# Optimization experiments

Hardware: AMD Instinct MI355X
Metric: run time of the kernel (lower is better)

## Reference

```python
import jax, jax.numpy as jnp
import numpy as np

B, S, D, H, DFF, NL, VOCAB, SRC = 16, 128, 768, 12, 3072, 6, 32000, 256


def _pe_table():
    pos = np.arange(S)[:, None].astype(np.float32)
    div = np.exp(np.arange(0, D, 2).astype(np.float32) * (-np.log(10000.0) / D))
    pe = np.zeros((S, D), np.float32)
    pe[:, 0::2] = np.sin(pos * div)
    pe[:, 1::2] = np.cos(pos * div)
    return jnp.asarray(pe)


def _ln(x, a, b, eps=1e-6):
    m = jnp.mean(x, axis=-1, keepdims=True)
    v = jnp.mean((x - m) ** 2, axis=-1, keepdims=True)
    return a * (x - m) / jnp.sqrt(v + eps) + b


def _mha(q_in, k_in, v_in, mask, Wq, bq, Wk, bk, Wv, bv, Wo, bo):
    Bq, Sq, Dm = q_in.shape
    Sk = k_in.shape[1]
    dk = Dm // H
    q = (q_in @ Wq + bq).reshape(Bq, Sq, H, dk).transpose(0, 2, 1, 3)
    k = (k_in @ Wk + bk).reshape(Bq, Sk, H, dk).transpose(0, 2, 1, 3)
    v = (v_in @ Wv + bv).reshape(Bq, Sk, H, dk).transpose(0, 2, 1, 3)
    s = jnp.einsum('bhqd,bhkd->bhqk', q, k) / jnp.sqrt(jnp.float32(dk))
    if mask is not None:
        s = jnp.where(mask == 0, jnp.float32(-1e9), s)
    a = jax.nn.softmax(s, axis=-1)
    o = jnp.einsum('bhqk,bhkd->bhqd', a, v).transpose(0, 2, 1, 3).reshape(Bq, Sq, Dm)
    return o @ Wo + bo


def _combined_mask(trg):
    # Vectorized, faithful replica of create_combined_mask (incl. its cumulative
    # cross-batch zeroing: for j in 0..B-2, if padding_start[j]!=0 zero rows
    # >= padding_start[j] of ALL batches b >= j).
    b, s = trg.shape
    is_pad = (trg == 0)
    haspad = jnp.any(is_pad, axis=1)
    start = jnp.where(haspad, jnp.argmax(is_pad, axis=1), 0)  # first pad idx, 0 if none
    c = jnp.where(start == 0, s + 1, start)                   # sentinel = never cut
    cmin = jax.lax.cummin(c)
    r = cmin[jnp.minimum(jnp.arange(b), b - 2)]               # effective cutoff per batch
    look = jnp.tril(jnp.ones((s, s), jnp.float32))
    keep = (jnp.arange(s)[None, :] < r[:, None]).astype(jnp.float32)  # (B,S) rows kept
    return (look[None] * keep[:, :, None])[:, None]           # (B,1,S,S)


def setup_inputs():
    key = jax.random.key(0)
    ks = jax.random.split(key, 16)
    tok = jax.random.randint(ks[0], (B, S), 1, VOCAB)
    lens = jax.random.randint(ks[1], (B,), S // 2, S + 1)
    trg = jnp.where(jnp.arange(S)[None, :] < lens[:, None], tok, 0).astype(jnp.int32)
    e_outputs = jax.random.normal(ks[2], (B, SRC, D), dtype=jnp.float32)
    src_mask = jax.random.randint(ks[3], (B, 1, 1, SRC), 0, 2).at[..., 0].set(1).astype(jnp.int32)
    w = lambda k, shape: (jax.random.normal(k, shape) * 0.02).astype(jnp.float32)
    emb = (jax.random.normal(ks[4], (VOCAB, D)) * 0.1).astype(jnp.float32).at[0].set(0.0)
    return {
        'trg': trg, 'e_outputs': e_outputs, 'src_mask': src_mask,
        'emb': emb,
        'y_param': jax.random.normal(ks[5], (S, D), dtype=jnp.float32),
        'pe_alpha': jnp.float32(1.0),
        'Wq': w(ks[6], (NL, 3, D, D)), 'Wk': w(ks[7], (NL, 3, D, D)),
        'Wv': w(ks[8], (NL, 3, D, D)), 'Wo': w(ks[9], (NL, 3, D, D)),
        'bq': jnp.zeros((NL, 3, D)), 'bk': jnp.zeros((NL, 3, D)),
        'bv': jnp.zeros((NL, 3, D)), 'bo': jnp.zeros((NL, 3, D)),
        'W1': w(ks[10], (NL, D, DFF)), 'b1': jnp.zeros((NL, DFF)),
        'W2': w(ks[11], (NL, DFF, D)), 'b2': jnp.zeros((NL, D)),
        'ln_a': jnp.ones((NL, 5, D)), 'ln_b': jnp.zeros((NL, 5, D)),
        'final_a': jnp.ones((D,)), 'final_b': jnp.zeros((D,)),
    }


def reference(trg, e_outputs, src_mask, emb, y_param, pe_alpha, Wq, Wk, Wv, Wo,
              bq, bk, bv, bo, W1, b1, W2, b2, ln_a, ln_b, final_a, final_b):
    x = emb[trg] + pe_alpha * _pe_table()            # embedding + scaled PE
    y = jnp.broadcast_to(y_param, (trg.shape[0],) + y_param.shape)
    trg_mask = _combined_mask(trg)
    for i in range(Wq.shape[0]):
        x2 = _ln(x, ln_a[i, 0], ln_b[i, 0])
        x = x + _mha(x2, x2, x2, trg_mask, Wq[i, 0], bq[i, 0], Wk[i, 0], bk[i, 0], Wv[i, 0], bv[i, 0], Wo[i, 0], bo[i, 0])
        y2 = _ln(y, ln_a[i, 1], ln_b[i, 1])
        y = y + _mha(y2, e_outputs, e_outputs, src_mask, Wq[i, 1], bq[i, 1], Wk[i, 1], bk[i, 1], Wv[i, 1], bv[i, 1], Wo[i, 1], bo[i, 1])
        x2 = _ln(x, ln_a[i, 2], ln_b[i, 2])
        y3 = _ln(y, ln_a[i, 3], ln_b[i, 3])
        x = x + _mha(x2, y3, y3, None, Wq[i, 2], bq[i, 2], Wk[i, 2], bk[i, 2], Wv[i, 2], bv[i, 2], Wo[i, 2], bo[i, 2])
        x2 = _ln(x, ln_a[i, 4], ln_b[i, 4])
        x = x + jnp.maximum(x2 @ W1[i] + b1[i], 0.0) @ W2[i] + b2[i]
    return _ln(x, final_a, final_b)
```

## Files before the change

kernel.cpp:

```cpp
#include <hip/hip_runtime.h>
#include <math.h>

#define BB 16
#define SS 128
#define DD 768
#define HH 12
#define DKK 64
#define DFFF 3072
#define NLL 6
#define SRCC 256

typedef short bf16x8 __attribute__((ext_vector_type(8)));
typedef float f32x4 __attribute__((ext_vector_type(4)));
typedef unsigned short us8 __attribute__((ext_vector_type(8)));
typedef unsigned short us4 __attribute__((ext_vector_type(4)));

__device__ __forceinline__ unsigned short f2bf(float f) {
  unsigned int u = __builtin_bit_cast(unsigned int, f);
  u = (u + 0x7fff + ((u >> 16) & 1)) >> 16;
  return (unsigned short)u;
}

#define GLOADLDS16(gp, lp)                                              \
  __builtin_amdgcn_global_load_lds(                                     \
      (const __attribute__((address_space(1))) void*)(gp),              \
      (__attribute__((address_space(3))) void*)(lp), 16, 0, 0)

__global__ void embjoint_k(const int* __restrict__ trg, const float* __restrict__ emb,
                           const float* __restrict__ alpha,
                           const float* __restrict__ yp,
                           float* __restrict__ x, float* __restrict__ y) {
  int idx = blockIdx.x * blockDim.x + threadIdx.x;
  int c = idx % (DD / 4);
  int r = idx / (DD / 4);
  if (r >= BB * SS) return;
  int s = r % SS;
  if (blockIdx.y == 0) {
    float al = alpha[0];
    float4 e = *(const float4*)(emb + (size_t)trg[r] * DD + c * 4);
    float coef = -logf(10000.0f) / (float)DD;
    float div0 = expf((float)(4 * c) * coef);
    float div1 = expf((float)(4 * c + 2) * coef);
    float s0, c0, s1, c1;
    sincosf((float)s * div0, &s0, &c0);
    sincosf((float)s * div1, &s1, &c1);
    float4 o;
    o.x = e.x + al * s0; o.y = e.y + al * c0;
    o.z = e.z + al * s1; o.w = e.w + al * c1;
    *(float4*)(x + (size_t)r * DD + c * 4) = o;
  } else {
    *(float4*)(y + (size_t)r * DD + c * 4) = *(const float4*)(yp + (size_t)s * DD + c * 4);
  }
}

__global__ void mb_k(const int* __restrict__ trg, int* __restrict__ rbuf,
                     const float* __restrict__ bq, const float* __restrict__ bk,
                     const float* __restrict__ bv, float* __restrict__ bqkv1,
                     float* __restrict__ bkv2, float* __restrict__ bqkv3) {
  int t = threadIdx.x;
  if (blockIdx.x == 0) {
    __shared__ int first[BB];
    if (t < BB) first[t] = 0x7fffffff;
    __syncthreads();
    int b = t >> 4, p0 = (t & 15) * 8;
    int loc = 0x7fffffff;
#pragma unroll
    for (int i = 0; i < 8; i++) {
      if (trg[b * SS + p0 + i] == 0) { loc = p0 + i; break; }
    }
    atomicMin(&first[b], loc);
    __syncthreads();
    if (t == 0) {
      int cmin = 0x7fffffff;
      int cm[BB];
      for (int bb = 0; bb < BB; bb++) {
        int start = (first[bb] == 0x7fffffff) ? 0 : first[bb];
        int c = (start == 0) ? (SS + 1) : start;
        cmin = min(cmin, c);
        cm[bb] = cmin;
      }
      for (int bb = 0; bb < BB; bb++) rbuf[bb] = cm[min(bb, BB - 2)];
    }
    return;
  }
  int i = (blockIdx.x - 1) * 256 + t;
  if (i >= NLL * 6144) return;
  int l = i / 6144, j = i - l * 6144;
  if (j < 2304) {
    int s = j / 768, c = j - s * 768;
    const float* src = (s == 0) ? bq : (s == 1 ? bk : bv);
    bqkv1[l * 2304 + j] = src[(l * 3 + 0) * 768 + c];
  } else if (j < 3840) {
    int jj = j - 2304;
    int s = jj / 768, c = jj - s * 768;
    bkv2[l * 1536 + jj] = ((s == 0) ? bk : bv)[(l * 3 + 1) * 768 + c];
  } else {
    int jj = j - 3840;
    int s = jj / 768, c = jj - s * 768;
    const float* src = (s == 0) ? bq : (s == 1 ? bk : bv);
    bqkv3[l * 2304 + jj] = src[(l * 3 + 2) * 768 + c];
  }
}

__global__ __launch_bounds__(256) void ln_k(const float* __restrict__ x,
                                            const float* __restrict__ ga,
                                            const float* __restrict__ gb,
                                            float* __restrict__ out) {
  __shared__ float sm[8];
  int row = blockIdx.x;
  int t = threadIdx.x;
  const float* xr = x + (size_t)row * DD;
  float v0 = xr[t], v1 = xr[t + 256], v2 = xr[t + 512];
  float s = v0 + v1 + v2;
#pragma unroll
  for (int o = 32; o > 0; o >>= 1) s += __shfl_down(s, o);
  if ((t & 63) == 0) sm[t >> 6] = s;
  __syncthreads();
  float mean = (sm[0] + sm[1] + sm[2] + sm[3]) * (1.0f / (float)DD);
  float d0 = v0 - mean, d1 = v1 - mean, d2 = v2 - mean;
  float q = d0 * d0 + d1 * d1 + d2 * d2;
#pragma unroll
  for (int o = 32; o > 0; o >>= 1) q += __shfl_down(q, o);
  if ((t & 63) == 0) sm[4 + (t >> 6)] = q;
  __syncthreads();
  float var = (sm[4] + sm[5] + sm[6] + sm[7]) * (1.0f / (float)DD);
  float inv = 1.0f / sqrtf(var + 1e-6f);
  float* orow = out + (size_t)row * DD;
  orow[t]       = ga[t] * d0 * inv + gb[t];
  orow[t + 256] = ga[t + 256] * d1 * inv + gb[t + 256];
  orow[t + 512] = ga[t + 512] * d2 * inv + gb[t + 512];
}

__device__ __forceinline__ void lnb_body(const float* __restrict__ xr,
                                         const float* __restrict__ ga,
                                         const float* __restrict__ gb,
                                         unsigned short* __restrict__ orow,
                                         float* sm, int t) {
  float v0 = xr[t], v1 = xr[t + 256], v2 = xr[t + 512];
  float s = v0 + v1 + v2;
#pragma unroll
  for (int o = 32; o > 0; o >>= 1) s += __shfl_down(s, o);
  if ((t & 63) == 0) sm[t >> 6] = s;
  __syncthreads();
  float mean = (sm[0] + sm[1] + sm[2] + sm[3]) * (1.0f / (float)DD);
  float d0 = v0 - mean, d1 = v1 - mean, d2 = v2 - mean;
  float q = d0 * d0 + d1 * d1 + d2 * d2;
#pragma unroll
  for (int o = 32; o > 0; o >>= 1) q += __shfl_down(q, o);
  if ((t & 63) == 0) sm[4 + (t >> 6)] = q;
  __syncthreads();
  float var = (sm[4] + sm[5] + sm[6] + sm[7]) * (1.0f / (float)DD);
  float inv = 1.0f / sqrtf(var + 1e-6f);
  orow[t]       = f2bf(ga[t] * d0 * inv + gb[t]);
  orow[t + 256] = f2bf(ga[t + 256] * d1 * inv + gb[t + 256]);
  orow[t + 512] = f2bf(ga[t + 512] * d2 * inv + gb[t + 512]);
}

__global__ __launch_bounds__(256) void lnb_k(const float* __restrict__ x,
                                             const float* __restrict__ ga,
                                             const float* __restrict__ gb,
                                             unsigned short* __restrict__ out) {
  __shared__ float sm[8];
  int row = blockIdx.x;
  lnb_body(x + (size_t)row * DD, ga, gb, out + (size_t)row * DD, sm, threadIdx.x);
}

__global__ __launch_bounds__(256) void lnb2_k(const float* __restrict__ x,
                                              const float* __restrict__ y,
                                              const float* __restrict__ gax,
                                              const float* __restrict__ gbx,
                                              const float* __restrict__ gay,
                                              const float* __restrict__ gby,
                                              unsigned short* __restrict__ ox,
                                              unsigned short* __restrict__ oy) {
  __shared__ float sm[8];
  int row = blockIdx.x;
  if (row < BB * SS)
    lnb_body(x + (size_t)row * DD, gax, gbx, ox + (size_t)row * DD, sm, threadIdx.x);
  else {
    row -= BB * SS;
    lnb_body(y + (size_t)row * DD, gay, gby, oy + (size_t)row * DD, sm, threadIdx.x);
  }
}

__device__ __forceinline__ void tr_tile(const float* __restrict__ s,
                                        unsigned short* __restrict__ d,
                                        int K, int N, int k0, int n0,
                                        float (*tl)[69], int t) {
#pragma unroll
  for (int i = 0; i < 8; i++) {
    int c = t + i * 256;
    int row = c >> 4, c4 = (c & 15) * 4;
    float4 v = *(const float4*)(s + (size_t)(k0 + row) * N + n0 + c4);
    tl[row][c4 + 0] = v.x; tl[row][c4 + 1] = v.y;
    tl[row][c4 + 2] = v.z; tl[row][c4 + 3] = v.w;
  }
  __syncthreads();
#pragma unroll
  for (int i = 0; i < 4; i++) {
    int c = t + i * 256;
    int n = c >> 4, kc = c & 15;
    us8 o;
#pragma unroll
    for (int j = 0; j < 8; j++) o[j] = f2bf(tl[kc * 8 + j][n]);
    *(us8*)(d + (size_t)(n0 + n) * K + k0 + kc * 8) = o;
  }
}

__global__ __launch_bounds__(256) void wtx_k(
    const float* __restrict__ Wq, const float* __restrict__ Wk,
    const float* __restrict__ Wv, const float* __restrict__ Wo,
    const float* __restrict__ W1, const float* __restrict__ W2,
    const float* __restrict__ e_out,
    unsigned short* __restrict__ wqkv1A, unsigned short* __restrict__ wq2A,
    unsigned short* __restrict__ wkv2A, unsigned short* __restrict__ wqkv3A,
    unsigned short* __restrict__ wotA,
    unsigned short* __restrict__ w1tA, unsigned short* __restrict__ w2tA,
    unsigned short* __restrict__ eob) {
  __shared__ float tl[128][69];
  const size_t M1 = (size_t)DD * DD;
  int bid = blockIdx.x;
  int t = threadIdx.x;
  if (bid < 5184) {
    int mat = bid / 72, rem = bid % 72;
    int kt = rem / 12, nt = rem % 12;
    int l = mat / 12, m = mat % 12;
    size_t s3 = (size_t)l * 3 * M1;
    const float* s;
    unsigned short* d;
    switch (m) {
      case 0:  s = Wq + s3;          d = wqkv1A + l * 3 * M1;          break;
      case 1:  s = Wk + s3;          d = wqkv1A + l * 3 * M1 + M1;     break;
      case 2:  s = Wv + s3;          d = wqkv1A + l * 3 * M1 + 2 * M1; break;
      case 3:  s = Wq + s3 + M1;     d = wq2A + l * M1;                break;
      case 4:  s = Wk + s3 + M1;     d = wkv2A + l * 2 * M1;           break;
      case 5:  s = Wv + s3 + M1;     d = wkv2A + l * 2 * M1 + M1;      break;
      case 6:  s = Wq + s3 + 2 * M1; d = wqkv3A + l * 3 * M1;          break;
      case 7:  s = Wk + s3 + 2 * M1; d = wqkv3A + l * 3 * M1 + M1;     break;
      case 8:  s = Wv + s3 + 2 * M1; d = wqkv3A + l * 3 * M1 + 2 * M1; break;
      case 9:  s = Wo + s3;          d = wotA + l * 3 * M1;            break;
      case 10: s = Wo + s3 + M1;     d = wotA + l * 3 * M1 + M1;       break;
      default: s = Wo + s3 + 2 * M1; d = wotA + l * 3 * M1 + 2 * M1;   break;
    }
    tr_tile(s, d, DD, DD, kt * 128, nt * 64, tl, t);
  } else if (bid < 6912) {
    int idx = bid - 5184;
    int l = idx / 288, rem = idx % 288;
    int kt = rem / 48, nt = rem % 48;
    tr_tile(W1 + (size_t)l * DD * DFFF, w1tA + (size_t)l * DD * DFFF,
            DD, DFFF, kt * 128, nt * 64, tl, t);
  } else if (bid < 8640) {
    int idx = bid - 6912;
    int l = idx / 288, rem = idx % 288;
    int kt = rem / 12, nt = rem % 12;
    tr_tile(W2 + (size_t)l * DFFF * DD, w2tA + (size_t)l * DFFF * DD,
            DFFF, DD, kt * 128, nt * 64, tl, t);
  } else {
    size_t base = (size_t)(bid - 8640) * 2048 + (size_t)t * 8;
    float4 a = *(const float4*)(e_out + base);
    float4 b = *(const float4*)(e_out + base + 4);
    us8 o;
    o[0] = f2bf(a.x); o[1] = f2bf(a.y); o[2] = f2bf(a.z); o[3] = f2bf(a.w);
    o[4] = f2bf(b.x); o[5] = f2bf(b.y); o[6] = f2bf(b.z); o[7] = f2bf(b.w);
    *(us8*)(eob + base) = o;
  }
}

#define GEMM_BODY(BM, A, Bt, m0, n0)                                          \
  constexpr int FM = (BM) / 32;                                               \
  constexpr int HB = (BM) / 2;                                                \
  int wave = t >> 6, lane = t & 63;                                           \
  int wm = wave >> 1, wn = wave & 1;                                          \
  f32x4 acc[FM][2] = {};                                                      \
  int aRow = t >> 2, aC8 = (t & 3) * 8;                                       \
  const unsigned short* Ab = (A) + (size_t)(m0)*768 + aC8;                    \
  const unsigned short* Bb = (Bt) + (size_t)(n0)*768 + aC8;                   \
  int aOff0 = (wm * HB + (lane & 15)) * 32 + (lane >> 4) * 8;                 \
  int bOff0 = (wn * 32 + (lane & 15)) * 32 + (lane >> 4) * 8;                 \
  for (int k0 = 0; k0 < 768; k0 += 32) {                                      \
    _Pragma("unroll")                                                         \
    for (int h = 0; h < (BM) / 64; h++)                                       \
      GLOADLDS16(Ab + (size_t)(h * 64 + aRow) * 768 + k0,                     \
                 As + h * 2048 + wave * 512);                                 \
    GLOADLDS16(Bb + (size_t)aRow * 768 + k0, Bs + wave * 512);                \
    __syncthreads();                                                          \
    bf16x8 aF[FM], bF[2];                                                     \
    _Pragma("unroll")                                                         \
    for (int fm = 0; fm < FM; fm++)                                           \
      aF[fm] = *(const bf16x8*)(As + aOff0 + fm * 16 * 32);                   \
    _Pragma("unroll")                                                         \
    for (int fn = 0; fn < 2; fn++)                                            \
      bF[fn] = *(const bf16x8*)(Bs + bOff0 + fn * 16 * 32);                   \
    _Pragma("unroll")                                                         \
    for (int fm = 0; fm < FM; fm++)                                           \
      _Pragma("unroll")                                                       \
      for (int fn = 0; fn < 2; fn++)                                          \
        acc[fm][fn] = __builtin_amdgcn_mfma_f32_16x16x32_bf16(                \
            aF[fm], bF[fn], acc[fm][fn], 0, 0, 0);                            \
    __syncthreads();                                                          \
  }                                                                           \
  int lcol = lane & 15, lrow4 = (lane >> 4) * 4;

__device__ __forceinline__ void hm_store(unsigned short* hd, int sh, int vt,
                                         int rowb, int colr, const f32x4& a,
                                         float bv) {
  int hh = colr >> 6, dd = colr & 63;
  int bb = rowb >> sh, ssb = rowb & ((1 << sh) - 1);
  if (vt) {
    size_t idx = (((size_t)bb * HH + hh) * 64 + dd) * (size_t)(1 << sh) + ssb;
    us4 pk;
#pragma unroll
    for (int r = 0; r < 4; r++) pk[r] = f2bf(a[r] + bv);
    *(us4*)(hd + idx) = pk;
  } else {
    size_t base = ((((size_t)bb * HH + hh) << sh) + ssb) * 64 + dd;
#pragma unroll
    for (int r = 0; r < 4; r++) hd[base + (size_t)r * 64] = f2bf(a[r] + bv);
  }
}

template <int BM>
__global__ __launch_bounds__(256) void mgemm_k(
    const unsigned short* __restrict__ A0, const unsigned short* __restrict__ A1,
    const unsigned short* __restrict__ Bt, const float* __restrict__ bias,
    const float* __restrict__ res, void* __restrict__ C,
    unsigned short* __restrict__ hd0, unsigned short* __restrict__ hd1,
    unsigned short* __restrict__ hd2,
    int sh0, int sh1, int sh2, int M, int N, int K, int flags, int vtbits) {
  constexpr int FM = BM / 32;
  constexpr int HB = BM / 2;
  __shared__ unsigned short As[BM * 32];
  __shared__ unsigned short Bs[64 * 32];
  int t = threadIdx.x;
  int wave = t >> 6, lane = t & 63;
  int m0 = blockIdx.y * BM, n0 = blockIdx.x * 64;
  int seg = n0 / 768;
  const unsigned short* A = (seg == 0) ? A0 : A1;
  int wm = wave >> 1, wn = wave & 1;
  f32x4 acc[FM][2] = {};
  int aRow = t >> 2, aC8 = (t & 3) * 8;
  const unsigned short* Ab = A + (size_t)m0 * K + aC8;
  const unsigned short* Bb = Bt + (size_t)n0 * K + aC8;
  int aOff0 = (wm * HB + (lane & 15)) * 32 + (lane >> 4) * 8;
  int bOff0 = (wn * 32 + (lane & 15)) * 32 + (lane >> 4) * 8;
  for (int k0 = 0; k0 < K; k0 += 32) {
#pragma unroll
    for (int h = 0; h < BM / 64; h++)
      GLOADLDS16(Ab + (size_t)(h * 64 + aRow) * K + k0, As + h * 2048 + wave * 512);
    GLOADLDS16(Bb + (size_t)aRow * K + k0, Bs + wave * 512);
    __syncthreads();
    bf16x8 aF[FM], bF[2];
#pragma unroll
    for (int fm = 0; fm < FM; fm++)
      aF[fm] = *(const bf16x8*)(As + aOff0 + fm * 16 * 32);
#pragma unroll
    for (int fn = 0; fn < 2; fn++)
      bF[fn] = *(const bf16x8*)(Bs + bOff0 + fn * 16 * 32);
#pragma unroll
    for (int fm = 0; fm < FM; fm++)
#pragma unroll
      for (int fn = 0; fn < 2; fn++)
        acc[fm][fn] = __builtin_amdgcn_mfma_f32_16x16x32_bf16(aF[fm], bF[fn], acc[fm][fn], 0, 0, 0);
    __syncthreads();
  }
  int lcol = lane & 15, lrow4 = (lane >> 4) * 4;
  bool hm = (flags & 4) != 0;
  unsigned short* hd = nullptr;
  int sh = 0, segBase = seg * 768, vtseg = 0;
  if (hm) {
    hd = (seg == 0) ? hd0 : (seg == 1 ? hd1 : hd2);
    sh = (seg == 0) ? sh0 : (seg == 1 ? sh1 : sh2);
    vtseg = (vtbits >> seg) & 1;
  }
#pragma unroll
  for (int fm = 0; fm < FM; fm++) {
#pragma unroll
    for (int fn = 0; fn < 2; fn++) {
      int col = n0 + wn * 32 + fn * 16 + lcol;
      float bv = bias[col];
      int rowb = m0 + wm * HB + fm * 16 + lrow4;
      if (hm) {
        hm_store(hd, sh, vtseg, rowb, col - segBase, acc[fm][fn], bv);
      } else {
#pragma unroll
        for (int r = 0; r < 4; r++) {
          int row = rowb + r;
          float v = acc[fm][fn][r] + bv;
          size_t idx = (size_t)row * N + col;
          if (res) v += res[idx];
          if (flags & 1) v = fmaxf(v, 0.f);
          if (flags & 2) ((unsigned short*)C)[idx] = f2bf(v);
          else ((float*)C)[idx] = v;
        }
      }
    }
  }
}

__global__ __launch_bounds__(256) void kv2all_k(
    const unsigned short* __restrict__ eob, const unsigned short* __restrict__ wkv2A,
    const float* __restrict__ bkv2,
    unsigned short* __restrict__ khb2A, unsigned short* __restrict__ vthb2A) {
  __shared__ unsigned short As[128 * 32];
  __shared__ unsigned short Bs[64 * 32];
  const size_t M1 = (size_t)DD * DD;
  const size_t KVS = (size_t)BB * HH * SRCC * DKK;
  int t = threadIdx.x;
  int l = blockIdx.z;
  int m0 = blockIdx.y * 128, n0 = blockIdx.x * 64;
  const unsigned short* Bt = wkv2A + (size_t)l * 2 * M1;
  const float* bias = bkv2 + l * 1536;
  GEMM_BODY(128, eob, Bt, m0, n0)
  int seg = n0 / 768;
  unsigned short* hd = (seg == 0) ? khb2A + (size_t)l * KVS : vthb2A + (size_t)l * KVS;
  int vt = seg;
  int segBase = seg * 768;
#pragma unroll
  for (int fm = 0; fm < FM; fm++) {
#pragma unroll
    for (int fn = 0; fn < 2; fn++) {
      int col = n0 + wn * 32 + fn * 16 + lcol;
      int rowb = m0 + wm * HB + fm * 16 + lrow4;
      hm_store(hd, 8, vt, rowb, col - segBase, acc[fm][fn], bias[col]);
    }
  }
}

__global__ __launch_bounds__(256) void qkvq_k(
    const unsigned short* __restrict__ x2b, const unsigned short* __restrict__ y1b,
    const unsigned short* __restrict__ Bqkv, const unsigned short* __restrict__ Bq2,
    const float* __restrict__ bias1, const float* __restrict__ bias2,
    unsigned short* __restrict__ qhb, unsigned short* __restrict__ khb,
    unsigned short* __restrict__ vthb, unsigned short* __restrict__ qhb2) {
  __shared__ unsigned short As[128 * 32];
  __shared__ unsigned short Bs[64 * 32];
  int t = threadIdx.x;
  int bid = blockIdx.x;
  bool j1 = bid >= 576;
  int bx, by;
  const unsigned short *A, *Bt;
  const float* bias;
  if (!j1) { bx = bid % 36; by = bid / 36; A = x2b; Bt = Bqkv; bias = bias1; }
  else { int b2 = bid - 576; bx = b2 % 12; by = b2 / 12; A = y1b; Bt = Bq2; bias = bias2; }
  int m0 = by * 128, n0 = bx * 64;
  GEMM_BODY(128, A, Bt, m0, n0)
  int seg = j1 ? 0 : (n0 / 768);
  unsigned short* hd = j1 ? qhb2 : (seg == 0 ? qhb : (seg == 1 ? khb : vthb));
  int vt = (!j1 && seg == 2) ? 1 : 0;
  int segBase = seg * 768;
#pragma unroll
  for (int fm = 0; fm < FM; fm++) {
#pragma unroll
    for (int fn = 0; fn < 2; fn++) {
      int col = n0 + wn * 32 + fn * 16 + lcol;
      int rowb = m0 + wm * HB + fm * 16 + lrow4;
      hm_store(hd, 7, vt, rowb, col - segBase, acc[fm][fn], bias[col]);
    }
  }
}

__global__ __launch_bounds__(256) void wob_k(
    const unsigned short* __restrict__ ctx1b, const unsigned short* __restrict__ ctx2b,
    const unsigned short* __restrict__ Bt0, const unsigned short* __restrict__ Bt1,
    const float* __restrict__ bo0, const float* __restrict__ bo1,
    float* __restrict__ x, float* __restrict__ y) {
  __shared__ unsigned short As[64 * 32];
  __shared__ unsigned short Bs[64 * 32];
  int t = threadIdx.x;
  int bid = blockIdx.x;
  bool j1 = bid >= 384;
  int b2 = j1 ? bid - 384 : bid;
  int bx = b2 % 12, by = b2 / 12;
  const unsigned short* A = j1 ? ctx2b : ctx1b;
  const unsigned short* Bt = j1 ? Bt1 : Bt0;
  const float* bias = j1 ? bo1 : bo0;
  float* C = j1 ? y : x;
  int m0 = by * 64, n0 = bx * 64;
  GEMM_BODY(64, A, Bt, m0, n0)
#pragma unroll
  for (int fm = 0; fm < FM; fm++) {
#pragma unroll
    for (int fn = 0; fn < 2; fn++) {
      int col = n0 + wn * 32 + fn * 16 + lcol;
      float bv = bias[col];
      int rowb = m0 + wm * HB + fm * 16 + lrow4;
#pragma unroll
      for (int r = 0; r < 4; r++) {
        size_t idx = (size_t)(rowb + r) * DD + col;
        C[idx] += acc[fm][fn][r] + bv;
      }
    }
  }
}

template <int SK>
__global__ __launch_bounds__(256) void attn3_k(const unsigned short* __restrict__ qh,
                                               const unsigned short* __restrict__ kh,
                                               const unsigned short* __restrict__ vth,
                                               unsigned short* __restrict__ ctxb, int mode,
                                               const int* __restrict__ rbuf,
                                               const int* __restrict__ smask) {
  constexpr int NPH = SK / 128;
  constexpr int NF = SK / 16;
  __shared__ unsigned short kvb[128 * 72];
  __shared__ unsigned short pbuf[64 * (SK + 8)];
  int qhalf = blockIdx.x, h = blockIdx.y, b = blockIdx.z;
  int t = threadIdx.x;
  int wave = t >> 6, lane = t & 63;
  int l15 = lane & 15, lhi = lane >> 4;
  int qrow0 = qhalf * 64 + wave * 16;
  size_t bh = (size_t)b * HH + h;
  bf16x8 aQ[2];
#pragma unroll
  for (int ks = 0; ks < 2; ks++)
    aQ[ks] = *(const bf16x8*)(qh + (bh * SS + qrow0 + l15) * 64 + ks * 32 + lhi * 8);
  f32x4 accS[NF] = {};
  const unsigned short* kbase = kh + bh * SK * 64;
  for (int ph = 0; ph < NPH; ph++) {
    if (ph) __syncthreads();
    {
      int c0 = t * 4;
#pragma unroll
      for (int i = 0; i < 4; i++) {
        int c = c0 + i, row = c >> 3, co = (c & 7) * 8;
        *(us8*)&kvb[row * 72 + co] = *(const us8*)(kbase + (size_t)(ph * 128 + row) * 64 + co);
      }
    }
    __syncthreads();
#pragma unroll
    for (int kf = 0; kf < 8; kf++) {
      int gf = ph * 8 + kf;
#pragma unroll
      for (int ks = 0; ks < 2; ks++) {
        bf16x8 bK = *(const bf16x8*)(&kvb[(kf * 16 + l15) * 72 + ks * 32 + lhi * 8]);
        accS[gf] = __builtin_amdgcn_mfma_f32_16x16x32_bf16(aQ[ks], bK, accS[gf], 0, 0, 0);
      }
    }
  }
  int rcut = (mode == 0) ? rbuf[b] : 0;
#pragma unroll
  for (int r = 0; r < 4; r++) {
    int qg = qrow0 + lhi * 4 + r;
    float mx = -3.4e38f;
#pragma unroll
    for (int gf = 0; gf < NF; gf++) {
      int k = gf * 16 + l15;
      float s = accS[gf][r] * 0.125f;
      bool keep = true;
      if (mode == 0) keep = (k <= qg) && (qg < rcut);
      else if (mode == 1) keep = (smask[b * SRCC + k] != 0);
      s = keep ? s : -1e9f;
      accS[gf][r] = s;
      mx = fmaxf(mx, s);
    }
#pragma unroll
    for (int o = 1; o < 16; o <<= 1) mx = fmaxf(mx, __shfl_xor(mx, o));
    float sum = 0.f;
#pragma unroll
    for (int gf = 0; gf < NF; gf++) {
      float e = expf(accS[gf][r] - mx);
      accS[gf][r] = e;
      sum += e;
    }
#pragma unroll
    for (int o = 1; o < 16; o <<= 1) sum += __shfl_xor(sum, o);
    float rinv = 1.0f / sum;
#pragma unroll
    for (int gf = 0; gf < NF; gf++) accS[gf][r] *= rinv;
  }
#pragma unroll
  for (int gf = 0; gf < NF; gf++) {
#pragma unroll
    for (int r = 0; r < 4; r++) {
      int ql = wave * 16 + lhi * 4 + r;
      pbuf[ql * (SK + 8) + gf * 16 + l15] = f2bf(accS[gf][r]);
    }
  }
  __syncthreads();
  f32x4 accO[4] = {};
  const unsigned short* vbase = vth + bh * 64 * SK;
  for (int ph = 0; ph < NPH; ph++) {
    if (ph) __syncthreads();
    {
      int c0 = t * 4;
#pragma unroll
      for (int i = 0; i < 4; i++) {
        int c = c0 + i, row = c >> 4, co = (c & 15) * 8;
        *(us8*)&kvb[row * 136 + co] = *(const us8*)(vbase + (size_t)row * SK + ph * 128 + co);
      }
    }
    __syncthreads();
#pragma unroll
    for (int ks = 0; ks < 4; ks++) {
      bf16x8 aP = *(const bf16x8*)(&pbuf[(wave * 16 + l15) * (SK + 8) + ph * 128 + ks * 32 + lhi * 8]);
#pragma unroll
      for (int nf = 0; nf < 4; nf++) {
        bf16x8 bV = *(const bf16x8*)(&kvb[(nf * 16 + l15) * 136 + ks * 32 + lhi * 8]);
        accO[nf] = __builtin_amdgcn_mfma_f32_16x16x32_bf16(aP, bV, accO[nf], 0, 0, 0);
      }
    }
  }
#pragma unroll
  for (int nf = 0; nf < 4; nf++) {
#pragma unroll
    for (int r = 0; r < 4; r++) {
      int qg = qrow0 + lhi * 4 + r;
      ctxb[((size_t)b * SS + qg) * DD + h * 64 + nf * 16 + l15] = f2bf(accO[nf][r]);
    }
  }
}

extern "C" void kernel_launch(void* const* d_in, const int* in_sizes, int n_in,
                              void* d_out, int out_size, void* d_ws, size_t ws_size,
                              hipStream_t stream) {
  const int*   trg   = (const int*)d_in[0];
  const float* e_out = (const float*)d_in[1];
  const int*   smask = (const int*)d_in[2];
  const float* emb   = (const float*)d_in[3];
  const float* ypar  = (const float*)d_in[4];
  const float* alpha = (const float*)d_in[5];
  const float* Wq = (const float*)d_in[6];
  const float* Wk = (const float*)d_in[7];
  const float* Wv = (const float*)d_in[8];
  const float* Wo = (const float*)d_in[9];
  const float* bq = (const float*)d_in[10];
  const float* bk = (const float*)d_in[11];
  const float* bv = (const float*)d_in[12];
  const float* bo = (const float*)d_in[13];
  const float* W1 = (const float*)d_in[14];
  const float* b1 = (const float*)d_in[15];
  const float* W2 = (const float*)d_in[16];
  const float* b2 = (const float*)d_in[17];
  const float* lna = (const float*)d_in[18];
  const float* lnbp = (const float*)d_in[19];
  const float* fa = (const float*)d_in[20];
  const float* fb = (const float*)d_in[21];
  float* out = (float*)d_out;

  float* ws = (float*)d_ws;
  size_t off = 0;
  auto alloc = [&](size_t n) { float* p = ws + off; off += n; return p; };
  const size_t M1 = (size_t)DD * DD;
  const size_t KVS = (size_t)BB * HH * SRCC * DKK;
  int* rbuf  = (int*)alloc(64);
  float* x   = alloc((size_t)BB * SS * DD);
  float* y   = alloc((size_t)BB * SS * DD);
  float* bqkv1 = alloc((size_t)NLL * 2304);
  float* bkv2  = alloc((size_t)NLL * 1536);
  float* bqkv3 = alloc((size_t)NLL * 2304);
  unsigned short* qhb   = (unsigned short*)alloc((size_t)BB * HH * SS * DKK / 2);
  unsigned short* qhb2  = (unsigned short*)alloc((size_t)BB * HH * SS * DKK / 2);
  unsigned short* khb   = (unsigned short*)alloc((size_t)BB * HH * SS * DKK / 2);
  unsigned short* vthb  = (unsigned short*)alloc((size_t)BB * HH * SS * DKK / 2);
  unsigned short* khb2A  = (unsigned short*)alloc((size_t)NLL * KVS / 2);
  unsigned short* vthb2A = (unsigned short*)alloc((size_t)NLL * KVS / 2);
  unsigned short* x2b   = (unsigned short*)alloc((size_t)BB * SS * DD / 2);
  unsigned short* y3b   = (unsigned short*)alloc((size_t)BB * SS * DD / 2);
  unsigned short* ctx1b = (unsigned short*)alloc((size_t)BB * SS * DD / 2);
  unsigned short* ctx2b = (unsigned short*)alloc((size_t)BB * SS * DD / 2);
  unsigned short* midb  = (unsigned short*)alloc((size_t)BB * SS * DFFF / 2);
  unsigned short* eob   = (unsigned short*)alloc((size_t)BB * SRCC * DD / 2);
  unsigned short* wqkv1A = (unsigned short*)alloc((size_t)NLL * 3 * M1 / 2);
  unsigned short* wq2A   = (unsigned short*)alloc((size_t)NLL * M1 / 2);
  unsigned short* wkv2A  = (unsigned short*)alloc((size_t)NLL * 2 * M1 / 2);
  unsigned short* wqkv3A = (unsigned short*)alloc((size_t)NLL * 3 * M1 / 2);
  unsigned short* wotA   = (unsigned short*)alloc((size_t)NLL * 3 * M1 / 2);
  unsigned short* w1tA   = (unsigned short*)alloc((size_t)NLL * DD * DFFF / 2);
  unsigned short* w2tA   = (unsigned short*)alloc((size_t)NLL * DFFF * DD / 2);
  if (ws_size < off * sizeof(float)) return;

  embjoint_k<<<dim3((BB * SS * (DD / 4) + 255) / 256, 2), 256, 0, stream>>>(
      trg, emb, alpha, ypar, x, y);
  mb_k<<<1 + (NLL * 6144 + 255) / 256, 256, 0, stream>>>(trg, rbuf, bq, bk, bv,
                                                         bqkv1, bkv2, bqkv3);
  wtx_k<<<10176, 256, 0, stream>>>(Wq, Wk, Wv, Wo, W1, W2, e_out,
                                   wqkv1A, wq2A, wkv2A, wqkv3A, wotA, w1tA, w2tA, eob);
  kv2all_k<<<dim3(24, 32, NLL), 256, 0, stream>>>(eob, wkv2A, bkv2, khb2A, vthb2A);

  auto MG128 = [&](const unsigned short* A0, const unsigned short* A1, int M, int K,
                   const unsigned short* Bt, int N, const float* bias, const float* res,
                   void* C, unsigned short* h0, unsigned short* h1, unsigned short* h2,
                   int s0, int s1, int s2, int flags, int vtb) {
    mgemm_k<128><<<dim3(N / 64, M / 128), 256, 0, stream>>>(A0, A1, Bt, bias, res, C,
                                                            h0, h1, h2, s0, s1, s2, M, N, K, flags, vtb);
  };
  auto MG64 = [&](const unsigned short* A0, int M, int K,
                  const unsigned short* Bt, int N, const float* bias, const float* res,
                  void* C, unsigned short* h0, int s0, int flags, int vtb) {
    mgemm_k<64><<<dim3(N / 64, M / 64), 256, 0, stream>>>(A0, A0, Bt, bias, res, C,
                                                          h0, nullptr, nullptr, s0, 0, 0, M, N, K, flags, vtb);
  };
  const dim3 agrid(SS / 64, HH, BB);

  for (int l = 0; l < NLL; l++) {
    const float* lA = lna + (size_t)l * 5 * DD;
    const float* lB = lnbp + (size_t)l * 5 * DD;
    lnb2_k<<<2 * BB * SS, 256, 0, stream>>>(x, y, lA, lB, lA + DD, lB + DD, x2b, y3b);
    qkvq_k<<<768, 256, 0, stream>>>(x2b, y3b, wqkv1A + l * 3 * M1, wq2A + l * M1,
                                    bqkv1 + l * 2304, bq + ((size_t)l * 3 + 1) * DD,
                                    qhb, khb, vthb, qhb2);
    attn3_k<SS><<<agrid, 256, 0, stream>>>(qhb, khb, vthb, ctx1b, 0, rbuf, nullptr);
    attn3_k<SRCC><<<agrid, 256, 0, stream>>>(qhb2, khb2A + l * KVS, vthb2A + l * KVS,
                                             ctx2b, 1, nullptr, smask);
    wob_k<<<768, 256, 0, stream>>>(ctx1b, ctx2b, wotA + l * 3 * M1, wotA + l * 3 * M1 + M1,
                                   bo + (size_t)l * 3 * DD, bo + ((size_t)l * 3 + 1) * DD, x, y);
    lnb2_k<<<2 * BB * SS, 256, 0, stream>>>(x, y, lA + 2 * DD, lB + 2 * DD,
                                            lA + 3 * DD, lB + 3 * DD, x2b, y3b);
    MG128(x2b, y3b, BB * SS, DD, wqkv3A + l * 3 * M1, 2304, bqkv3 + l * 2304, nullptr,
          nullptr, qhb, khb, vthb, 7, 7, 7, 4, 0b100);
    attn3_k<SS><<<agrid, 256, 0, stream>>>(qhb, khb, vthb, ctx1b, 2, nullptr, nullptr);
    MG64(ctx1b, BB * SS, DD, wotA + l * 3 * M1 + 2 * M1, DD, bo + ((size_t)l * 3 + 2) * DD,
         x, x, nullptr, 0, 0, 0);
    lnb_k<<<BB * SS, 256, 0, stream>>>(x, lA + 4 * DD, lB + 4 * DD, x2b);
    MG128(x2b, x2b, BB * SS, DD, w1tA + (size_t)l * DD * DFFF, DFFF, b1 + (size_t)l * DFFF,
          nullptr, midb, nullptr, nullptr, nullptr, 0, 0, 0, 3, 0);
    MG64(midb, BB * SS, DFFF, w2tA + (size_t)l * DFFF * DD, DD, b2 + (size_t)l * DD, x, x,
         nullptr, 0, 0, 0);
  }
  ln_k<<<BB * SS, 256, 0, stream>>>(x, fa, fb, out);
}
```

Baseline: 1.529 ms.

## Fuse self and cross attention launches, shrink transpose tiles, remap kv2 grid

The per-layer causal self-attention and cross-attention kernels are merged into one launch of 768 blocks. The longer cross-attention blocks come first, which removes a launch per layer and lets the two run concurrently. The weight-transpose prep kernel now uses 64x64 tiles, which doubles the block count and halves LDS use per block for better occupancy. The cross-KV GEMM moves to a flat 1D grid with an XCD-aware swizzle for better L2 locality. As a trade-off, the fused attention kernel always reserves the larger SK=256 LDS footprint, even for self-attention blocks.

```diff
diff --git a/kernel.cpp b/kernel.cpp
--- a/kernel.cpp
+++ b/kernel.cpp
@@ -183,12 +183,12 @@
   }
 }
 
-__device__ __forceinline__ void tr_tile(const float* __restrict__ s,
-                                        unsigned short* __restrict__ d,
-                                        int K, int N, int k0, int n0,
-                                        float (*tl)[69], int t) {
-#pragma unroll
-  for (int i = 0; i < 8; i++) {
+__device__ __forceinline__ void tr_tile64(const float* __restrict__ s,
+                                          unsigned short* __restrict__ d,
+                                          int K, int N, int k0, int n0,
+                                          float (*tl)[69], int t) {
+#pragma unroll
+  for (int i = 0; i < 4; i++) {
     int c = t + i * 256;
     int row = c >> 4, c4 = (c & 15) * 4;
     float4 v = *(const float4*)(s + (size_t)(k0 + row) * N + n0 + c4);
@@ -197,9 +197,9 @@
   }
   __syncthreads();
 #pragma unroll
-  for (int i = 0; i < 4; i++) {
+  for (int i = 0; i < 2; i++) {
     int c = t + i * 256;
-    int n = c >> 4, kc = c & 15;
+    int n = c >> 3, kc = c & 7;
     us8 o;
 #pragma unroll
     for (int j = 0; j < 8; j++) o[j] = f2bf(tl[kc * 8 + j][n]);
@@ -217,12 +217,12 @@
     unsigned short* __restrict__ wotA,
     unsigned short* __restrict__ w1tA, unsigned short* __restrict__ w2tA,
     unsigned short* __restrict__ eob) {
-  __shared__ float tl[128][69];
+  __shared__ float tl[64][69];
   const size_t M1 = (size_t)DD * DD;
   int bid = blockIdx.x;
   int t = threadIdx.x;
-  if (bid < 5184) {
-    int mat = bid / 72, rem = bid % 72;
+  if (bid < 10368) {
+    int mat = bid / 144, rem = bid % 144;
     int kt = rem / 12, nt = rem % 12;
     int l = mat / 12, m = mat % 12;
     size_t s3 = (size_t)l * 3 * M1;
@@ -242,21 +242,21 @@
       case 10: s = Wo + s3 + M1;     d = wotA + l * 3 * M1 + M1;       break;
       default: s = Wo + s3 + 2 * M1; d = wotA + l * 3 * M1 + 2 * M1;   break;
     }
-    tr_tile(s, d, DD, DD, kt * 128, nt * 64, tl, t);
-  } else if (bid < 6912) {
-    int idx = bid - 5184;
-    int l = idx / 288, rem = idx % 288;
+    tr_tile64(s, d, DD, DD, kt * 64, nt * 64, tl, t);
+  } else if (bid < 13824) {
+    int idx = bid - 10368;
+    int l = idx / 576, rem = idx % 576;
     int kt = rem / 48, nt = rem % 48;
-    tr_tile(W1 + (size_t)l * DD * DFFF, w1tA + (size_t)l * DD * DFFF,
-            DD, DFFF, kt * 128, nt * 64, tl, t);
-  } else if (bid < 8640) {
-    int idx = bid - 6912;
-    int l = idx / 288, rem = idx % 288;
+    tr_tile64(W1 + (size_t)l * DD * DFFF, w1tA + (size_t)l * DD * DFFF,
+              DD, DFFF, kt * 64, nt * 64, tl, t);
+  } else if (bid < 17280) {
+    int idx = bid - 13824;
+    int l = idx / 576, rem = idx % 576;
     int kt = rem / 12, nt = rem % 12;
-    tr_tile(W2 + (size_t)l * DFFF * DD, w2tA + (size_t)l * DFFF * DD,
-            DFFF, DD, kt * 128, nt * 64, tl, t);
+    tr_tile64(W2 + (size_t)l * DFFF * DD, w2tA + (size_t)l * DFFF * DD,
+              DFFF, DD, kt * 64, nt * 64, tl, t);
   } else {
-    size_t base = (size_t)(bid - 8640) * 2048 + (size_t)t * 8;
+    size_t base = (size_t)(bid - 17280) * 2048 + (size_t)t * 8;
     float4 a = *(const float4*)(e_out + base);
     float4 b = *(const float4*)(e_out + base + 4);
     us8 o;
@@ -406,14 +406,18 @@
   const size_t M1 = (size_t)DD * DD;
   const size_t KVS = (size_t)BB * HH * SRCC * DKK;
   int t = threadIdx.x;
-  int l = blockIdx.z;
-  int m0 = blockIdx.y * 128, n0 = blockIdx.x * 64;
+  int flat = blockIdx.x;
+  int nf = (flat & 7) * 576 + (flat >> 3);
+  int bx = nf % 24;
+  int rem = nf / 24;
+  int by = rem & 31;
+  int l = rem >> 5;
+  int m0 = by * 128, n0 = bx * 64;
   const unsigned short* Bt = wkv2A + (size_t)l * 2 * M1;
   const float* bias = bkv2 + l * 1536;
   GEMM_BODY(128, eob, Bt, m0, n0)
   int seg = n0 / 768;
   unsigned short* hd = (seg == 0) ? khb2A + (size_t)l * KVS : vthb2A + (size_t)l * KVS;
-  int vt = seg;
   int segBase = seg * 768;
 #pragma unroll
   for (int fm = 0; fm < FM; fm++) {
@@ -421,7 +425,7 @@
     for (int fn = 0; fn < 2; fn++) {
       int col = n0 + wn * 32 + fn * 16 + lcol;
       int rowb = m0 + wm * HB + fm * 16 + lrow4;
-      hm_store(hd, 8, vt, rowb, col - segBase, acc[fm][fn], bias[col]);
+      hm_store(hd, 8, seg, rowb, col - segBase, acc[fm][fn], bias[col]);
     }
   }
 }
@@ -494,17 +498,14 @@
 }
 
 template <int SK>
-__global__ __launch_bounds__(256) void attn3_k(const unsigned short* __restrict__ qh,
-                                               const unsigned short* __restrict__ kh,
-                                               const unsigned short* __restrict__ vth,
-                                               unsigned short* __restrict__ ctxb, int mode,
-                                               const int* __restrict__ rbuf,
-                                               const int* __restrict__ smask) {
+__device__ __forceinline__ void attn_body(
+    const unsigned short* __restrict__ qh, const unsigned short* __restrict__ kh,
+    const unsigned short* __restrict__ vth, unsigned short* __restrict__ ctxb,
+    int mode, const int* __restrict__ rbuf, const int* __restrict__ smask,
+    unsigned short* __restrict__ kvb, unsigned short* __restrict__ pbuf,
+    int qhalf, int h, int b) {
   constexpr int NPH = SK / 128;
   constexpr int NF = SK / 16;
-  __shared__ unsigned short kvb[128 * 72];
-  __shared__ unsigned short pbuf[64 * (SK + 8)];
-  int qhalf = blockIdx.x, h = blockIdx.y, b = blockIdx.z;
   int t = threadIdx.x;
   int wave = t >> 6, lane = t & 63;
   int l15 = lane & 15, lhi = lane >> 4;
@@ -607,6 +608,41 @@
       int qg = qrow0 + lhi * 4 + r;
       ctxb[((size_t)b * SS + qg) * DD + h * 64 + nf * 16 + l15] = f2bf(accO[nf][r]);
     }
+  }
+}
+
+template <int SK>
+__global__ __launch_bounds__(256) void attn3_k(const unsigned short* __restrict__ qh,
+                                               const unsigned short* __restrict__ kh,
+                                               const unsigned short* __restrict__ vth,
+                                               unsigned short* __restrict__ ctxb, int mode,
+                                               const int* __restrict__ rbuf,
+                                               const int* __restrict__ smask) {
+  __shared__ unsigned short kvb[128 * 72];
+  __shared__ unsigned short pbuf[64 * (SK + 8)];
+  attn_body<SK>(qh, kh, vth, ctxb, mode, rbuf, smask, kvb, pbuf,
+                blockIdx.x, blockIdx.y, blockIdx.z);
+}
+
+__global__ __launch_bounds__(256) void attnboth_k(
+    const unsigned short* __restrict__ qh1, const unsigned short* __restrict__ kh1,
+    const unsigned short* __restrict__ vth1,
+    const unsigned short* __restrict__ qh2, const unsigned short* __restrict__ kh2,
+    const unsigned short* __restrict__ vth2,
+    unsigned short* __restrict__ ctx1b, unsigned short* __restrict__ ctx2b,
+    const int* __restrict__ rbuf, const int* __restrict__ smask) {
+  __shared__ unsigned short kvb[128 * 72];
+  __shared__ unsigned short pbuf[64 * (SRCC + 8)];
+  int bid = blockIdx.x;
+  if (bid < 384) {
+    int qhalf = bid & 1, rest = bid >> 1;
+    int h = rest % HH, b = rest / HH;
+    attn_body<SRCC>(qh2, kh2, vth2, ctx2b, 1, nullptr, smask, kvb, pbuf, qhalf, h, b);
+  } else {
+    int b2 = bid - 384;
+    int qhalf = b2 & 1, rest = b2 >> 1;
+    int h = rest % HH, b = rest / HH;
+    attn_body<SS>(qh1, kh1, vth1, ctx1b, 0, rbuf, nullptr, kvb, pbuf, qhalf, h, b);
   }
 }
 
@@ -673,9 +709,9 @@
       trg, emb, alpha, ypar, x, y);
   mb_k<<<1 + (NLL * 6144 + 255) / 256, 256, 0, stream>>>(trg, rbuf, bq, bk, bv,
                                                          bqkv1, bkv2, bqkv3);
-  wtx_k<<<10176, 256, 0, stream>>>(Wq, Wk, Wv, Wo, W1, W2, e_out,
+  wtx_k<<<18816, 256, 0, stream>>>(Wq, Wk, Wv, Wo, W1, W2, e_out,
                                    wqkv1A, wq2A, wkv2A, wqkv3A, wotA, w1tA, w2tA, eob);
-  kv2all_k<<<dim3(24, 32, NLL), 256, 0, stream>>>(eob, wkv2A, bkv2, khb2A, vthb2A);
+  kv2all_k<<<4608, 256, 0, stream>>>(eob, wkv2A, bkv2, khb2A, vthb2A);
 
   auto MG128 = [&](const unsigned short* A0, const unsigned short* A1, int M, int K,
                    const unsigned short* Bt, int N, const float* bias, const float* res,
@@ -699,9 +735,9 @@
     qkvq_k<<<768, 256, 0, stream>>>(x2b, y3b, wqkv1A + l * 3 * M1, wq2A + l * M1,
                                     bqkv1 + l * 2304, bq + ((size_t)l * 3 + 1) * DD,
                                     qhb, khb, vthb, qhb2);
-    attn3_k<SS><<<agrid, 256, 0, stream>>>(qhb, khb, vthb, ctx1b, 0, rbuf, nullptr);
-    attn3_k<SRCC><<<agrid, 256, 0, stream>>>(qhb2, khb2A + l * KVS, vthb2A + l * KVS,
-                                             ctx2b, 1, nullptr, smask);
+    attnboth_k<<<768, 256, 0, stream>>>(qhb, khb, vthb,
+                                        qhb2, khb2A + l * KVS, vthb2A + l * KVS,
+                                        ctx1b, ctx2b, rbuf, smask);
     wob_k<<<768, 256, 0, stream>>>(ctx1b, ctx2b, wotA + l * 3 * M1, wotA + l * 3 * M1 + M1,
                                    bo + (size_t)l * 3 * DD, bo + ((size_t)l * 3 + 1) * DD, x, y);
     lnb2_k<<<2 * BB * SS, 256, 0, stream>>>(x, y, lA + 2 * DD, lB + 2 * DD,
```

Result: faster. 1.447 ms (-5.4%).
